# Optimization experiments

Measured on AMD Instinct MI355X. Metric: run time of the kernel, lower is better.

The kernel has to match this reference:

```python
import jax, jax.numpy as jnp
import numpy as np

B, S, H, F, E, K = 8, 4096, 256, 512, 16, 2
EPS = 1e-5


def setup_inputs() -> dict:
    key = jax.random.key(0)
    ks = jax.random.split(key, 9)
    sc = 0.02
    return {
        "x": jax.random.normal(ks[0], (B, S, H), dtype=jnp.float32),
        "gate_w": jax.random.normal(ks[1], (H, E), dtype=jnp.float32) * sc,
        "gate_b": jnp.zeros((E,), dtype=jnp.float32),
        "w1": jax.random.normal(ks[2], (E, H, F), dtype=jnp.float32) * sc,
        "b1": jnp.zeros((E, F), dtype=jnp.float32),
        "w2": jax.random.normal(ks[3], (E, F, H), dtype=jnp.float32) * sc,
        "b2": jnp.zeros((E, H), dtype=jnp.float32),
        "gamma": jnp.ones((H,), dtype=jnp.float32),
        "beta": jnp.zeros((H,), dtype=jnp.float32),
    }


def reference(x, gate_w, gate_b, w1, b1, w2, b2, gamma, beta):
    # gating: top-k over expert logits, softmax over the k selected logits
    gate_logits = x @ gate_w + gate_b                      # [B,S,E]
    topk_vals, topk_idx = jax.lax.top_k(gate_logits, K)    # [B,S,K]
    topk_w = jax.nn.softmax(topk_vals, axis=-1)            # [B,S,K]

    # naive dense MoE: every expert runs over every token (matches source)
    h = jax.nn.relu(jnp.einsum('bsh,ehf->bsef', x, w1) + b1)   # [B,S,E,F]
    expert_out = jnp.einsum('bsef,efh->bseh', h, w2) + b2       # [B,S,E,H]

    # select top-k expert outputs and combine with gate weights
    sel = jnp.take_along_axis(expert_out, topk_idx[:, :, :, None], axis=2)  # [B,S,K,H]
    moe = jnp.sum(topk_w[..., None] * sel, axis=2)              # [B,S,H]

    # residual + LayerNorm
    y = x + moe
    mu = jnp.mean(y, axis=-1, keepdims=True)
    var = jnp.var(y, axis=-1, keepdims=True)
    return (y - mu) / jnp.sqrt(var + EPS) * gamma + beta
```

## Files before the change

kernel.cpp:

```cpp
#include <hip/hip_runtime.h>
#include <hip/hip_bf16.h>

typedef __bf16 bf16_t;
typedef __bf16 bf16x8 __attribute__((ext_vector_type(8)));
typedef __bf16 bf16x4 __attribute__((ext_vector_type(4)));
typedef float f32x4 __attribute__((ext_vector_type(4)));

#define NB 8
#define NS 4096
#define NH 256
#define NF 512
#define NE 16
#define NTOK (NB*NS)
#define TT 64
#define NCH 16
#define HS_STRIDE 40

__device__ __forceinline__ void load_lds16(const void* g, void* l) {
    __builtin_amdgcn_global_load_lds(
        (const __attribute__((address_space(1))) unsigned int*)g,
        (__attribute__((address_space(3))) unsigned int*)l, 16, 0, 0);
}

__global__ __launch_bounds__(256) void transpose_kernel(
    const float* __restrict__ w1, const float* __restrict__ w2,
    bf16_t* __restrict__ w1t, bf16_t* __restrict__ w2t)
{
    __shared__ float tile[32][33];
    int bid = blockIdx.x;
    const float* src; bf16_t* dst; int R, C; int isw1;
    if (bid < 2048) { src = w1; dst = w1t; R = NH; C = NF; isw1 = 1; }
    else            { bid -= 2048; src = w2; dst = w2t; R = NF; C = NH; isw1 = 0; }
    int e = bid >> 7;
    int t = bid & 127;
    int tcols = C / 32;
    int tr = (t / tcols) * 32, tc = (t % tcols) * 32;
    src += (size_t)e * R * C;
    dst += (size_t)e * R * C;
    int tx = threadIdx.x & 31, ty0 = threadIdx.x >> 5;
    #pragma unroll
    for (int i = 0; i < 4; i++) {
        int ty = ty0 + i * 8;
        tile[ty][tx] = src[(size_t)(tr + ty) * C + tc + tx];
    }
    __syncthreads();
    if (threadIdx.x < 128) {
        int j = threadIdx.x & 31;
        int g = threadIdx.x >> 5;
        bf16x8 v;
        #pragma unroll
        for (int jj = 0; jj < 8; jj++)
            v[jj] = (bf16_t)tile[g * 8 + jj][j];
        size_t idx;
        if (isw1) {
            int f  = tc + j;
            int kb = tr + g * 8;
            idx = (size_t)f * NH + ((((kb >> 3) ^ (f & 7))) << 3);
        } else {
            int h  = tc + j;
            int fb = tr + g * 8;
            idx = ((size_t)(fb >> 5) * NH + h) * 32 + (fb & 31);
        }
        *(bf16x8*)(dst + idx) = v;
    }
}

__global__ __launch_bounds__(256) void gate_kernel(
    const float* __restrict__ x, const float* __restrict__ gate_w,
    const float* __restrict__ gate_b,
    int* __restrict__ counts, int* __restrict__ bucket_enc,
    float* __restrict__ bucket_gw, bf16_t* __restrict__ xb)
{
    __shared__ float gws[NH][NE];
    __shared__ int lcnt[NE];
    __shared__ int gbase[NE];

    for (int i = threadIdx.x; i < NH * NE; i += 256)
        gws[i >> 4][i & 15] = gate_w[i];
    if (threadIdx.x < NE) lcnt[threadIdx.x] = 0;
    __syncthreads();

    int tok = blockIdx.x * 256 + threadIdx.x;
    const float4* xr = (const float4*)(x + (size_t)tok * NH);
    bf16x4* xbr = (bf16x4*)(xb + (size_t)tok * NH);
    float acc[NE];
    #pragma unroll
    for (int e = 0; e < NE; e++) acc[e] = gate_b[e];
    for (int h4 = 0; h4 < NH / 4; h4++) {
        float4 xv = xr[h4];
        bf16x4 xo;
        xo[0] = (bf16_t)xv.x; xo[1] = (bf16_t)xv.y;
        xo[2] = (bf16_t)xv.z; xo[3] = (bf16_t)xv.w;
        xbr[h4] = xo;
        #pragma unroll
        for (int j = 0; j < 4; j++) {
            float xs = (j == 0) ? xv.x : (j == 1) ? xv.y : (j == 2) ? xv.z : xv.w;
            int h = h4 * 4 + j;
            #pragma unroll
            for (int e = 0; e < NE; e++) acc[e] += xs * gws[h][e];
        }
    }
    float v0 = -1e30f, v1 = -1e30f; int i0 = 0, i1 = 0;
    #pragma unroll
    for (int e = 0; e < NE; e++) {
        float a = acc[e];
        if (a > v0)      { v1 = v0; i1 = i0; v0 = a; i0 = e; }
        else if (a > v1) { v1 = a; i1 = e; }
    }
    float e1 = __expf(v1 - v0);
    float s  = 1.f + e1;
    int   pe[2] = { i0, i1 };
    float pg[2] = { 1.f / s, e1 / s };
    int   po[2];
    po[0] = atomicAdd(&lcnt[i0], 1);
    po[1] = atomicAdd(&lcnt[i1], 1);
    __syncthreads();
    if (threadIdx.x < NE)
        gbase[threadIdx.x] = atomicAdd(&counts[threadIdx.x], lcnt[threadIdx.x]);
    __syncthreads();
    #pragma unroll
    for (int k = 0; k < 2; k++) {
        int e = pe[k];
        int pos = gbase[e] + po[k];
        bucket_enc[e * NTOK + pos] = tok | (k << 20);
        bucket_gw [e * NTOK + pos] = pg[k];
    }
}

__global__ __launch_bounds__(256, 3) void moe_kernel(
    const bf16_t* __restrict__ xb,
    const bf16_t* __restrict__ w1t,
    const float*  __restrict__ b1,
    const bf16_t* __restrict__ w2t,
    const float*  __restrict__ b2,
    const int* __restrict__ counts,
    const int* __restrict__ bucket_enc,
    const float* __restrict__ bucket_gw,
    bf16_t* __restrict__ pairbuf)
{
    __shared__ uint4 W1s4[2][1024];
    __shared__ __align__(16) bf16_t Hs[2][TT][HS_STRIDE];
    __shared__ int   tok_s[TT];
    __shared__ float gw_s[TT];

    int flat = blockIdx.x;
    int xcd  = flat & 7;
    int j    = flat >> 3;
    int e    = xcd * 2 + (j & 1);
    int tile0 = j >> 1;
    int n_e = counts[e];
    int wave = threadIdx.x >> 6;
    int lane = threadIdx.x & 63;
    int l15 = lane & 15, q = lane >> 4;

    const bf16_t* w1te = w1t + (size_t)e * NF * NH;
    const bf16_t* w2te = w2t + (size_t)e * NF * NH;

    int ntiles = (n_e + TT - 1) / TT;
    for (int tile = tile0; tile < ntiles; tile += 48) {
        int tstart = tile * TT;
        __syncthreads();
        if (threadIdx.x < TT) {
            int slot = tstart + threadIdx.x;
            if (slot < n_e) {
                tok_s[threadIdx.x] = bucket_enc[e * NTOK + slot];
                gw_s [threadIdx.x] = bucket_gw [e * NTOK + slot];
            } else { tok_s[threadIdx.x] = 0; gw_s[threadIdx.x] = 0.f; }
        }
        __syncthreads();

        {
            const uint4* gw1 = (const uint4*)w1te;
            #pragma unroll
            for (int i = 0; i < 4; i++)
                load_lds16(gw1 + i * 256 + threadIdx.x, &W1s4[0][i * 256 + threadIdx.x]);
        }
        int mytok = tok_s[wave * 16 + l15] & 0xFFFFF;
        const uint4* xrow = (const uint4*)(xb + (size_t)mytok * NH);
        uint4 xf[8];
        #pragma unroll
        for (int ks = 0; ks < 8; ks++) xf[ks] = xrow[ks * 4 + q];
        __syncthreads();

        f32x4 oacc[4][4];
        #pragma unroll
        for (int a = 0; a < 4; a++)
            #pragma unroll
            for (int b = 0; b < 4; b++) { f32x4 z = {0.f,0.f,0.f,0.f}; oacc[a][b] = z; }

        for (int ch = 0; ch < NCH; ch++) {
            int buf = ch & 1;
            if (ch + 1 < NCH) {
                const uint4* gw1 = (const uint4*)w1te + (size_t)(ch + 1) * 1024;
                #pragma unroll
                for (int i = 0; i < 4; i++)
                    load_lds16(gw1 + i * 256 + threadIdx.x,
                               &W1s4[buf ^ 1][i * 256 + threadIdx.x]);
            }
            bf16x8 bf2[4];
            #pragma unroll
            for (int nt = 0; nt < 4; nt++) {
                int hh = wave * 64 + nt * 16 + l15;
                bf2[nt] = *(const bf16x8*)&w2te[(((size_t)ch * NH + hh) << 5) + q * 8];
            }
            f32x4 hacc[2]; { f32x4 z = {0.f,0.f,0.f,0.f}; hacc[0] = z; hacc[1] = z; }
            const bf16_t* w1s = (const bf16_t*)W1s4[buf];
            #pragma unroll
            for (int ks = 0; ks < 8; ks++) {
                bf16x8 xfrag = *(const bf16x8*)&xf[ks];
                #pragma unroll
                for (int n = 0; n < 2; n++) {
                    int fl = n * 16 + l15;
                    bf16x8 wf = *(const bf16x8*)&w1s[fl * NH + ((((ks * 4 + q) ^ (fl & 7))) << 3)];
                    hacc[n] = __builtin_amdgcn_mfma_f32_16x16x32_bf16(wf, xfrag, hacc[n], 0, 0, 0);
                }
            }
            #pragma unroll
            for (int n = 0; n < 2; n++) {
                int f0 = ch * 32 + n * 16 + q * 4;
                float4 b1v = *(const float4*)&b1[e * NF + f0];
                bf16x4 hv;
                #pragma unroll
                for (int r = 0; r < 4; r++) {
                    float v = hacc[n][r] + ((const float*)&b1v)[r];
                    v = v > 0.f ? v : 0.f;
                    hv[r] = (bf16_t)v;
                }
                *(bf16x4*)&Hs[buf][wave * 16 + l15][n * 16 + q * 4] = hv;
            }
            __syncthreads();
            #pragma unroll
            for (int mt = 0; mt < 4; mt++) {
                bf16x8 hf = *(const bf16x8*)&Hs[buf][mt * 16 + l15][q * 8];
                #pragma unroll
                for (int nt = 0; nt < 4; nt++) {
                    oacc[mt][nt] = __builtin_amdgcn_mfma_f32_16x16x32_bf16(bf2[nt], hf, oacc[mt][nt], 0, 0, 0);
                }
            }
        }
        int nrows = n_e - tstart; if (nrows > TT) nrows = TT;
        float4 b2v[4];
        #pragma unroll
        for (int nt = 0; nt < 4; nt++)
            b2v[nt] = *(const float4*)&b2[e * NH + wave * 64 + nt * 16 + q * 4];
        #pragma unroll
        for (int mt = 0; mt < 4; mt++) {
            int trow = mt * 16 + l15;
            int enc  = tok_s[trow];
            float gw = gw_s[trow];
            bool valid = trow < nrows;
            int tok = enc & 0xFFFFF;
            int kk  = enc >> 20;
            bf16_t* orow = pairbuf + ((size_t)(tok * 2 + kk)) * NH;
            #pragma unroll
            for (int nt = 0; nt < 4; nt++) {
                int col = wave * 64 + nt * 16 + q * 4;
                bf16x4 ov;
                #pragma unroll
                for (int r = 0; r < 4; r++)
                    ov[r] = (bf16_t)((oacc[mt][nt][r] + ((const float*)&b2v[nt])[r]) * gw);
                if (valid) *(bf16x4*)&orow[col] = ov;
            }
        }
    }
}

__global__ __launch_bounds__(256) void ln_kernel(
    const float* __restrict__ x, const bf16_t* __restrict__ pairbuf,
    const float* __restrict__ gamma, const float* __restrict__ beta,
    float* __restrict__ out)
{
    int tok  = blockIdx.x * 4 + (threadIdx.x >> 6);
    int lane = threadIdx.x & 63;
    float4 xv = *(const float4*)(x + (size_t)tok * NH + lane * 4);
    bf16x4 p0 = *(const bf16x4*)(pairbuf + (size_t)(tok * 2)     * NH + lane * 4);
    bf16x4 p1 = *(const bf16x4*)(pairbuf + (size_t)(tok * 2 + 1) * NH + lane * 4);
    float y0 = xv.x + (float)p0[0] + (float)p1[0];
    float y1 = xv.y + (float)p0[1] + (float)p1[1];
    float y2 = xv.z + (float)p0[2] + (float)p1[2];
    float y3 = xv.w + (float)p0[3] + (float)p1[3];
    float s  = y0 + y1 + y2 + y3;
    float s2 = y0 * y0 + y1 * y1 + y2 * y2 + y3 * y3;
    #pragma unroll
    for (int o = 32; o > 0; o >>= 1) {
        s  += __shfl_xor(s, o);
        s2 += __shfl_xor(s2, o);
    }
    float mu   = s * (1.f / NH);
    float var  = s2 * (1.f / NH) - mu * mu;
    float rstd = rsqrtf(var + 1e-5f);
    float4 gv = *(const float4*)(gamma + lane * 4);
    float4 bv = *(const float4*)(beta  + lane * 4);
    float4 o4;
    o4.x = (y0 - mu) * rstd * gv.x + bv.x;
    o4.y = (y1 - mu) * rstd * gv.y + bv.y;
    o4.z = (y2 - mu) * rstd * gv.z + bv.z;
    o4.w = (y3 - mu) * rstd * gv.w + bv.w;
    *(float4*)(out + (size_t)tok * NH + lane * 4) = o4;
}

extern "C" void kernel_launch(void* const* d_in, const int* in_sizes, int n_in,
                              void* d_out, int out_size, void* d_ws, size_t ws_size,
                              hipStream_t stream) {
    const float* x      = (const float*)d_in[0];
    const float* gate_w = (const float*)d_in[1];
    const float* gate_b = (const float*)d_in[2];
    const float* w1     = (const float*)d_in[3];
    const float* b1     = (const float*)d_in[4];
    const float* w2     = (const float*)d_in[5];
    const float* b2     = (const float*)d_in[6];
    const float* gamma  = (const float*)d_in[7];
    const float* beta   = (const float*)d_in[8];
    float* out = (float*)d_out;

    char* ws = (char*)d_ws;
    const size_t MB = 1024 * 1024;
    int*    counts     = (int*)ws;
    int*    bucket_enc = (int*)(ws + 256);
    float*  bucket_gw  = (float*)(ws + 256 + 2 * MB);
    bf16_t* w1t        = (bf16_t*)(ws + 256 + 4 * MB);
    bf16_t* w2t        = (bf16_t*)(ws + 256 + 8 * MB);
    bf16_t* xb         = (bf16_t*)(ws + 256 + 12 * MB);
    bf16_t* pairbuf    = (bf16_t*)(ws + 256 + 28 * MB);

    hipMemsetAsync(counts, 0, 256, stream);
    transpose_kernel<<<4096, 256, 0, stream>>>(w1, w2, w1t, w2t);
    gate_kernel<<<128, 256, 0, stream>>>(x, gate_w, gate_b, counts, bucket_enc, bucket_gw, xb);
    moe_kernel<<<768, 256, 0, stream>>>(xb, w1t, b1, w2t, b2, counts, bucket_enc, bucket_gw, pairbuf);
    ln_kernel<<<NTOK / 4, 256, 0, stream>>>(x, pairbuf, gamma, beta, out);
}
```

Measured before the change: 249.0 us.

## Prefetch W2 fragments, stage MoE output via LDS, widen grid, drop gate LDS

The MoE kernel now loads the next chunk's W2 fragments one iteration early into registers, overlapping that global load with the current chunk's MFMAs. The epilogue writes results through a swizzled LDS staging buffer (reusing the W1 buffer) so each token row is stored as full 16-byte coalesced rows instead of scattered 8-byte writes. The grid grows from 768 to 1024 blocks (64 tiles per expert stride) for more parallelism. The gate kernel also reads gate_w straight from global memory (cached) instead of staging it in LDS. These changes cost extra registers, which may lower occupancy, and add a sync in the epilogue.

```diff
diff --git a/kernel.cpp b/kernel.cpp
--- a/kernel.cpp
+++ b/kernel.cpp
@@ -71,12 +71,8 @@
     int* __restrict__ counts, int* __restrict__ bucket_enc,
     float* __restrict__ bucket_gw, bf16_t* __restrict__ xb)
 {
-    __shared__ float gws[NH][NE];
     __shared__ int lcnt[NE];
     __shared__ int gbase[NE];
-
-    for (int i = threadIdx.x; i < NH * NE; i += 256)
-        gws[i >> 4][i & 15] = gate_w[i];
     if (threadIdx.x < NE) lcnt[threadIdx.x] = 0;
     __syncthreads();
 
@@ -95,9 +91,9 @@
         #pragma unroll
         for (int j = 0; j < 4; j++) {
             float xs = (j == 0) ? xv.x : (j == 1) ? xv.y : (j == 2) ? xv.z : xv.w;
-            int h = h4 * 4 + j;
-            #pragma unroll
-            for (int e = 0; e < NE; e++) acc[e] += xs * gws[h][e];
+            const float* wr = gate_w + (h4 * 4 + j) * NE;
+            #pragma unroll
+            for (int e = 0; e < NE; e++) acc[e] += xs * wr[e];
         }
     }
     float v0 = -1e30f, v1 = -1e30f; int i0 = 0, i1 = 0;
@@ -144,10 +140,8 @@
     __shared__ float gw_s[TT];
 
     int flat = blockIdx.x;
-    int xcd  = flat & 7;
-    int j    = flat >> 3;
-    int e    = xcd * 2 + (j & 1);
-    int tile0 = j >> 1;
+    int e    = (flat & 7) * 2 + ((flat >> 3) & 1);
+    int tile0 = flat >> 4;
     int n_e = counts[e];
     int wave = threadIdx.x >> 6;
     int lane = threadIdx.x & 63;
@@ -157,7 +151,7 @@
     const bf16_t* w2te = w2t + (size_t)e * NF * NH;
 
     int ntiles = (n_e + TT - 1) / TT;
-    for (int tile = tile0; tile < ntiles; tile += 48) {
+    for (int tile = tile0; tile < ntiles; tile += 64) {
         int tstart = tile * TT;
         __syncthreads();
         if (threadIdx.x < TT) {
@@ -180,6 +174,12 @@
         uint4 xf[8];
         #pragma unroll
         for (int ks = 0; ks < 8; ks++) xf[ks] = xrow[ks * 4 + q];
+        bf16x8 bf2c[4], bf2n[4];
+        #pragma unroll
+        for (int nt = 0; nt < 4; nt++) {
+            int hh = wave * 64 + nt * 16 + l15;
+            bf2c[nt] = *(const bf16x8*)&w2te[((size_t)hh << 5) + q * 8];
+        }
         __syncthreads();
 
         f32x4 oacc[4][4];
@@ -190,18 +190,18 @@
 
         for (int ch = 0; ch < NCH; ch++) {
             int buf = ch & 1;
-            if (ch + 1 < NCH) {
+            bool have_next = (ch + 1 < NCH);
+            if (have_next) {
                 const uint4* gw1 = (const uint4*)w1te + (size_t)(ch + 1) * 1024;
                 #pragma unroll
                 for (int i = 0; i < 4; i++)
                     load_lds16(gw1 + i * 256 + threadIdx.x,
                                &W1s4[buf ^ 1][i * 256 + threadIdx.x]);
-            }
-            bf16x8 bf2[4];
-            #pragma unroll
-            for (int nt = 0; nt < 4; nt++) {
-                int hh = wave * 64 + nt * 16 + l15;
-                bf2[nt] = *(const bf16x8*)&w2te[(((size_t)ch * NH + hh) << 5) + q * 8];
+                #pragma unroll
+                for (int nt = 0; nt < 4; nt++) {
+                    int hh = wave * 64 + nt * 16 + l15;
+                    bf2n[nt] = *(const bf16x8*)&w2te[(((size_t)(ch + 1) * NH + hh) << 5) + q * 8];
+                }
             }
             f32x4 hacc[2]; { f32x4 z = {0.f,0.f,0.f,0.f}; hacc[0] = z; hacc[1] = z; }
             const bf16_t* w1s = (const bf16_t*)W1s4[buf];
@@ -234,32 +234,52 @@
                 bf16x8 hf = *(const bf16x8*)&Hs[buf][mt * 16 + l15][q * 8];
                 #pragma unroll
                 for (int nt = 0; nt < 4; nt++) {
-                    oacc[mt][nt] = __builtin_amdgcn_mfma_f32_16x16x32_bf16(bf2[nt], hf, oacc[mt][nt], 0, 0, 0);
-                }
-            }
-        }
-        int nrows = n_e - tstart; if (nrows > TT) nrows = TT;
-        float4 b2v[4];
-        #pragma unroll
-        for (int nt = 0; nt < 4; nt++)
-            b2v[nt] = *(const float4*)&b2[e * NH + wave * 64 + nt * 16 + q * 4];
-        #pragma unroll
-        for (int mt = 0; mt < 4; mt++) {
-            int trow = mt * 16 + l15;
-            int enc  = tok_s[trow];
-            float gw = gw_s[trow];
-            bool valid = trow < nrows;
-            int tok = enc & 0xFFFFF;
-            int kk  = enc >> 20;
-            bf16_t* orow = pairbuf + ((size_t)(tok * 2 + kk)) * NH;
-            #pragma unroll
-            for (int nt = 0; nt < 4; nt++) {
-                int col = wave * 64 + nt * 16 + q * 4;
-                bf16x4 ov;
-                #pragma unroll
-                for (int r = 0; r < 4; r++)
-                    ov[r] = (bf16_t)((oacc[mt][nt][r] + ((const float*)&b2v[nt])[r]) * gw);
-                if (valid) *(bf16x4*)&orow[col] = ov;
+                    oacc[mt][nt] = __builtin_amdgcn_mfma_f32_16x16x32_bf16(bf2c[nt], hf, oacc[mt][nt], 0, 0, 0);
+                }
+            }
+            if (have_next) {
+                #pragma unroll
+                for (int nt = 0; nt < 4; nt++) bf2c[nt] = bf2n[nt];
+            }
+        }
+        {
+            bf16_t* stage = (bf16_t*)W1s4;
+            float4 b2v[4];
+            #pragma unroll
+            for (int nt = 0; nt < 4; nt++)
+                b2v[nt] = *(const float4*)&b2[e * NH + wave * 64 + nt * 16 + q * 4];
+            #pragma unroll
+            for (int mt = 0; mt < 4; mt++) {
+                int row = mt * 16 + l15;
+                float gw = gw_s[row];
+                #pragma unroll
+                for (int nt = 0; nt < 4; nt++) {
+                    int unit = wave * 8 + nt * 2 + (q >> 1);
+                    int su = unit ^ (row & 7);
+                    bf16x4 ov;
+                    #pragma unroll
+                    for (int r = 0; r < 4; r++)
+                        ov[r] = (bf16_t)((oacc[mt][nt][r] + ((const float*)&b2v[nt])[r]) * gw);
+                    *(bf16x4*)&stage[row * NH + su * 8 + (q & 1) * 4] = ov;
+                }
+            }
+        }
+        __syncthreads();
+        {
+            const uint4* stage4 = &W1s4[0][0];
+            int nrows = n_e - tstart; if (nrows > TT) nrows = TT;
+            int c  = threadIdx.x & 31;
+            int r0 = threadIdx.x >> 5;
+            #pragma unroll
+            for (int i = 0; i < 8; i++) {
+                int r = r0 + i * 8;
+                if (r < nrows) {
+                    int enc = tok_s[r];
+                    int tok = enc & 0xFFFFF;
+                    int k   = enc >> 20;
+                    ((uint4*)(pairbuf + ((size_t)(tok * 2 + k)) * NH))[c] =
+                        stage4[r * 32 + (c ^ (r & 7))];
+                }
             }
         }
     }
@@ -326,6 +346,6 @@
     hipMemsetAsync(counts, 0, 256, stream);
     transpose_kernel<<<4096, 256, 0, stream>>>(w1, w2, w1t, w2t);
     gate_kernel<<<128, 256, 0, stream>>>(x, gate_w, gate_b, counts, bucket_enc, bucket_gw, xb);
-    moe_kernel<<<768, 256, 0, stream>>>(xb, w1t, b1, w2t, b2, counts, bucket_enc, bucket_gw, pairbuf);
+    moe_kernel<<<1024, 256, 0, stream>>>(xb, w1t, b1, w2t, b2, counts, bucket_enc, bucket_gw, pairbuf);
     ln_kernel<<<NTOK / 4, 256, 0, stream>>>(x, pairbuf, gamma, beta, out);
 }
```

Result: no change. 249.1 us (+0.0%).

## Fuse gate into transpose kernel and prefetch W2 fragments one chunk ahead

Applied to the files above, without the earlier changes.

The gate/top-k routing and the weight transpose now run as one prep kernel, so the tiny gate grid overlaps with the transpose blocks and one launch is saved. In the MoE kernel, the W2 fragments for the next chunk are loaded a chunk early into registers, and the full barriers are replaced with explicit vmcnt/lgkmcnt waits plus s_barrier. The b1/b2 biases are staged in LDS. Hand-written waitcnt values are fragile, and the gate path now reads gate_w from global memory instead of LDS.

```diff
diff --git a/kernel.cpp b/kernel.cpp
--- a/kernel.cpp
+++ b/kernel.cpp
@@ -22,12 +22,71 @@
         (__attribute__((address_space(3))) unsigned int*)l, 16, 0, 0);
 }
 
-__global__ __launch_bounds__(256) void transpose_kernel(
+__global__ __launch_bounds__(256) void prep_kernel(
     const float* __restrict__ w1, const float* __restrict__ w2,
-    bf16_t* __restrict__ w1t, bf16_t* __restrict__ w2t)
+    bf16_t* __restrict__ w1t, bf16_t* __restrict__ w2t,
+    const float* __restrict__ x, const float* __restrict__ gate_w,
+    const float* __restrict__ gate_b,
+    int* __restrict__ counts, int* __restrict__ bucket_enc,
+    float* __restrict__ bucket_gw, bf16_t* __restrict__ xb)
 {
     __shared__ float tile[32][33];
-    int bid = blockIdx.x;
+    __shared__ int lcnt[NE];
+    __shared__ int gbase[NE];
+
+    if (blockIdx.x < 128) {
+        if (threadIdx.x < NE) lcnt[threadIdx.x] = 0;
+        __syncthreads();
+
+        int tok = blockIdx.x * 256 + threadIdx.x;
+        const float4* xr = (const float4*)(x + (size_t)tok * NH);
+        bf16x4* xbr = (bf16x4*)(xb + (size_t)tok * NH);
+        float acc[NE];
+        #pragma unroll
+        for (int e = 0; e < NE; e++) acc[e] = gate_b[e];
+        for (int h4 = 0; h4 < NH / 4; h4++) {
+            float4 xv = xr[h4];
+            bf16x4 xo;
+            xo[0] = (bf16_t)xv.x; xo[1] = (bf16_t)xv.y;
+            xo[2] = (bf16_t)xv.z; xo[3] = (bf16_t)xv.w;
+            xbr[h4] = xo;
+            #pragma unroll
+            for (int j = 0; j < 4; j++) {
+                float xs = (j == 0) ? xv.x : (j == 1) ? xv.y : (j == 2) ? xv.z : xv.w;
+                const float* wr = gate_w + (h4 * 4 + j) * NE;
+                #pragma unroll
+                for (int e = 0; e < NE; e++) acc[e] += xs * wr[e];
+            }
+        }
+        float v0 = -1e30f, v1 = -1e30f; int i0 = 0, i1 = 0;
+        #pragma unroll
+        for (int e = 0; e < NE; e++) {
+            float a = acc[e];
+            if (a > v0)      { v1 = v0; i1 = i0; v0 = a; i0 = e; }
+            else if (a > v1) { v1 = a; i1 = e; }
+        }
+        float e1 = __expf(v1 - v0);
+        float s  = 1.f + e1;
+        int   pe[2] = { i0, i1 };
+        float pg[2] = { 1.f / s, e1 / s };
+        int   po[2];
+        po[0] = atomicAdd(&lcnt[i0], 1);
+        po[1] = atomicAdd(&lcnt[i1], 1);
+        __syncthreads();
+        if (threadIdx.x < NE)
+            gbase[threadIdx.x] = atomicAdd(&counts[threadIdx.x], lcnt[threadIdx.x]);
+        __syncthreads();
+        #pragma unroll
+        for (int k = 0; k < 2; k++) {
+            int e = pe[k];
+            int pos = gbase[e] + po[k];
+            bucket_enc[e * NTOK + pos] = tok | (k << 20);
+            bucket_gw [e * NTOK + pos] = pg[k];
+        }
+        return;
+    }
+
+    int bid = blockIdx.x - 128;
     const float* src; bf16_t* dst; int R, C; int isw1;
     if (bid < 2048) { src = w1; dst = w1t; R = NH; C = NF; isw1 = 1; }
     else            { bid -= 2048; src = w2; dst = w2t; R = NF; C = NH; isw1 = 0; }
@@ -62,68 +121,6 @@
             idx = ((size_t)(fb >> 5) * NH + h) * 32 + (fb & 31);
         }
         *(bf16x8*)(dst + idx) = v;
-    }
-}
-
-__global__ __launch_bounds__(256) void gate_kernel(
-    const float* __restrict__ x, const float* __restrict__ gate_w,
-    const float* __restrict__ gate_b,
-    int* __restrict__ counts, int* __restrict__ bucket_enc,
-    float* __restrict__ bucket_gw, bf16_t* __restrict__ xb)
-{
-    __shared__ float gws[NH][NE];
-    __shared__ int lcnt[NE];
-    __shared__ int gbase[NE];
-
-    for (int i = threadIdx.x; i < NH * NE; i += 256)
-        gws[i >> 4][i & 15] = gate_w[i];
-    if (threadIdx.x < NE) lcnt[threadIdx.x] = 0;
-    __syncthreads();
-
-    int tok = blockIdx.x * 256 + threadIdx.x;
-    const float4* xr = (const float4*)(x + (size_t)tok * NH);
-    bf16x4* xbr = (bf16x4*)(xb + (size_t)tok * NH);
-    float acc[NE];
-    #pragma unroll
-    for (int e = 0; e < NE; e++) acc[e] = gate_b[e];
-    for (int h4 = 0; h4 < NH / 4; h4++) {
-        float4 xv = xr[h4];
-        bf16x4 xo;
-        xo[0] = (bf16_t)xv.x; xo[1] = (bf16_t)xv.y;
-        xo[2] = (bf16_t)xv.z; xo[3] = (bf16_t)xv.w;
-        xbr[h4] = xo;
-        #pragma unroll
-        for (int j = 0; j < 4; j++) {
-            float xs = (j == 0) ? xv.x : (j == 1) ? xv.y : (j == 2) ? xv.z : xv.w;
-            int h = h4 * 4 + j;
-            #pragma unroll
-            for (int e = 0; e < NE; e++) acc[e] += xs * gws[h][e];
-        }
-    }
-    float v0 = -1e30f, v1 = -1e30f; int i0 = 0, i1 = 0;
-    #pragma unroll
-    for (int e = 0; e < NE; e++) {
-        float a = acc[e];
-        if (a > v0)      { v1 = v0; i1 = i0; v0 = a; i0 = e; }
-        else if (a > v1) { v1 = a; i1 = e; }
-    }
-    float e1 = __expf(v1 - v0);
-    float s  = 1.f + e1;
-    int   pe[2] = { i0, i1 };
-    float pg[2] = { 1.f / s, e1 / s };
-    int   po[2];
-    po[0] = atomicAdd(&lcnt[i0], 1);
-    po[1] = atomicAdd(&lcnt[i1], 1);
-    __syncthreads();
-    if (threadIdx.x < NE)
-        gbase[threadIdx.x] = atomicAdd(&counts[threadIdx.x], lcnt[threadIdx.x]);
-    __syncthreads();
-    #pragma unroll
-    for (int k = 0; k < 2; k++) {
-        int e = pe[k];
-        int pos = gbase[e] + po[k];
-        bucket_enc[e * NTOK + pos] = tok | (k << 20);
-        bucket_gw [e * NTOK + pos] = pg[k];
     }
 }
 
@@ -142,6 +139,8 @@
     __shared__ __align__(16) bf16_t Hs[2][TT][HS_STRIDE];
     __shared__ int   tok_s[TT];
     __shared__ float gw_s[TT];
+    __shared__ float b1_s[NF];
+    __shared__ float b2_s[NH];
 
     int flat = blockIdx.x;
     int xcd  = flat & 7;
@@ -156,6 +155,12 @@
     const bf16_t* w1te = w1t + (size_t)e * NF * NH;
     const bf16_t* w2te = w2t + (size_t)e * NF * NH;
 
+    if (threadIdx.x < 256) {
+        b1_s[threadIdx.x]       = b1[e * NF + threadIdx.x];
+        b1_s[threadIdx.x + 256] = b1[e * NF + threadIdx.x + 256];
+        b2_s[threadIdx.x]       = b2[e * NH + threadIdx.x];
+    }
+
     int ntiles = (n_e + TT - 1) / TT;
     for (int tile = tile0; tile < ntiles; tile += 48) {
         int tstart = tile * TT;
@@ -180,6 +185,12 @@
         uint4 xf[8];
         #pragma unroll
         for (int ks = 0; ks < 8; ks++) xf[ks] = xrow[ks * 4 + q];
+        bf16x8 bf2c[4], bf2n[4];
+        #pragma unroll
+        for (int nt = 0; nt < 4; nt++) {
+            int hh = wave * 64 + nt * 16 + l15;
+            bf2c[nt] = *(const bf16x8*)&w2te[((size_t)hh << 5) + q * 8];
+        }
         __syncthreads();
 
         f32x4 oacc[4][4];
@@ -196,13 +207,18 @@
                 for (int i = 0; i < 4; i++)
                     load_lds16(gw1 + i * 256 + threadIdx.x,
                                &W1s4[buf ^ 1][i * 256 + threadIdx.x]);
-            }
-            bf16x8 bf2[4];
-            #pragma unroll
-            for (int nt = 0; nt < 4; nt++) {
-                int hh = wave * 64 + nt * 16 + l15;
-                bf2[nt] = *(const bf16x8*)&w2te[(((size_t)ch * NH + hh) << 5) + q * 8];
-            }
+                #pragma unroll
+                for (int nt = 0; nt < 4; nt++) {
+                    int hh = wave * 64 + nt * 16 + l15;
+                    bf2n[nt] = *(const bf16x8*)&w2te[(((size_t)(ch + 1) * NH + hh) << 5) + q * 8];
+                }
+                asm volatile("s_waitcnt vmcnt(12)" ::: "memory");
+            } else {
+                asm volatile("s_waitcnt vmcnt(4)" ::: "memory");
+            }
+            __builtin_amdgcn_s_barrier();
+            __builtin_amdgcn_sched_barrier(0);
+
             f32x4 hacc[2]; { f32x4 z = {0.f,0.f,0.f,0.f}; hacc[0] = z; hacc[1] = z; }
             const bf16_t* w1s = (const bf16_t*)W1s4[buf];
             #pragma unroll
@@ -218,7 +234,7 @@
             #pragma unroll
             for (int n = 0; n < 2; n++) {
                 int f0 = ch * 32 + n * 16 + q * 4;
-                float4 b1v = *(const float4*)&b1[e * NF + f0];
+                float4 b1v = *(const float4*)&b1_s[f0];
                 bf16x4 hv;
                 #pragma unroll
                 for (int r = 0; r < 4; r++) {
@@ -228,21 +244,28 @@
                 }
                 *(bf16x4*)&Hs[buf][wave * 16 + l15][n * 16 + q * 4] = hv;
             }
-            __syncthreads();
+            asm volatile("s_waitcnt lgkmcnt(0)" ::: "memory");
+            __builtin_amdgcn_s_barrier();
+            __builtin_amdgcn_sched_barrier(0);
+
             #pragma unroll
             for (int mt = 0; mt < 4; mt++) {
                 bf16x8 hf = *(const bf16x8*)&Hs[buf][mt * 16 + l15][q * 8];
                 #pragma unroll
                 for (int nt = 0; nt < 4; nt++) {
-                    oacc[mt][nt] = __builtin_amdgcn_mfma_f32_16x16x32_bf16(bf2[nt], hf, oacc[mt][nt], 0, 0, 0);
+                    oacc[mt][nt] = __builtin_amdgcn_mfma_f32_16x16x32_bf16(bf2c[nt], hf, oacc[mt][nt], 0, 0, 0);
                 }
+            }
+            if (ch + 1 < NCH) {
+                #pragma unroll
+                for (int nt = 0; nt < 4; nt++) bf2c[nt] = bf2n[nt];
             }
         }
         int nrows = n_e - tstart; if (nrows > TT) nrows = TT;
         float4 b2v[4];
         #pragma unroll
         for (int nt = 0; nt < 4; nt++)
-            b2v[nt] = *(const float4*)&b2[e * NH + wave * 64 + nt * 16 + q * 4];
+            b2v[nt] = *(const float4*)&b2_s[wave * 64 + nt * 16 + q * 4];
         #pragma unroll
         for (int mt = 0; mt < 4; mt++) {
             int trow = mt * 16 + l15;
@@ -324,8 +347,9 @@
     bf16_t* pairbuf    = (bf16_t*)(ws + 256 + 28 * MB);
 
     hipMemsetAsync(counts, 0, 256, stream);
-    transpose_kernel<<<4096, 256, 0, stream>>>(w1, w2, w1t, w2t);
-    gate_kernel<<<128, 256, 0, stream>>>(x, gate_w, gate_b, counts, bucket_enc, bucket_gw, xb);
+    prep_kernel<<<4224, 256, 0, stream>>>(w1, w2, w1t, w2t,
+                                          x, gate_w, gate_b,
+                                          counts, bucket_enc, bucket_gw, xb);
     moe_kernel<<<768, 256, 0, stream>>>(xb, w1t, b1, w2t, b2, counts, bucket_enc, bucket_gw, pairbuf);
     ln_kernel<<<NTOK / 4, 256, 0, stream>>>(x, pairbuf, gamma, beta, out);
 }
```

New measurement: 233.2 us. 1.07x faster.
